# Optimization experiments

Hardware: AMD Instinct MI355X
Metric: run time of the kernel (lower is better)

## Reference

```python
import jax, jax.numpy as jnp
import numpy as np

C = 256
LN_EPS = 1e-5

def setup_inputs() -> dict:
    key = jax.random.key(0)
    ks = jax.random.split(key, 12)
    B, M, N = 8, 4096, 4096
    scale = 1.0 / np.sqrt(C)
    inp = {
        'x': jax.random.normal(ks[0], (B, M, C), jnp.float32),
        'y': jax.random.normal(ks[1], (B, N, C), jnp.float32),
        'Wq': jax.random.normal(ks[2], (C, C), jnp.float32) * scale,
        'bq': jnp.zeros((C,), jnp.float32),
        'Wk': jax.random.normal(ks[3], (C, C), jnp.float32) * scale,
        'bk': jnp.zeros((C,), jnp.float32),
        'Wv': jax.random.normal(ks[4], (C, C), jnp.float32) * scale,
        'bv': jnp.zeros((C,), jnp.float32),
        'Wo': jax.random.normal(ks[5], (C, C), jnp.float32) * (scale * 1e-5),
        'bo': jnp.zeros((C,), jnp.float32),
        'gamma': jnp.ones((C,), jnp.float32),
        'beta': jnp.zeros((C,), jnp.float32),
    }
    return inp

def reference(x, y, Wq, bq, Wk, bk, Wv, bv, Wo, bo, gamma, beta):
    # projections (torch Linear: x @ W.T + b)
    q = x @ Wq.T + bq                      # [B,M,C]
    k = y @ Wk.T + bk                      # [B,N,C]
    v = y @ Wv.T + bv                      # [B,N,C]
    # scaled dot-product attention with explicit score matrix
    w = jnp.einsum('bmc,bnc->bmn', q, k) * (C ** -0.5)  # [B,M,N]
    w = jax.nn.softmax(w, axis=-1)
    h = jnp.einsum('bmn,bnc->bmc', w, v)   # [B,M,C]
    h = h @ Wo.T + bo
    z = x + h
    # LayerNorm over last dim
    mu = jnp.mean(z, axis=-1, keepdims=True)
    var = jnp.var(z, axis=-1, keepdims=True)
    out = (z - mu) * jax.lax.rsqrt(var + LN_EPS) * gamma + beta
    return out
```

## Files before the change

### kernel.cpp

```cpp
#include <hip/hip_runtime.h>
#include <hip/hip_bf16.h>

#define C_DIM 256
#define QSCALE 0.09016844f
#define SM_BIAS -6.0f
#define WO_SCALE 1048576.0f
#define WO_INV   9.5367431640625e-07f

typedef __attribute__((ext_vector_type(8))) short bf16x8;
typedef __attribute__((ext_vector_type(4))) float f32x4;
typedef __attribute__((ext_vector_type(16))) float f32x16;

__device__ __forceinline__ void gload16(const unsigned char* g, unsigned char* l) {
    __builtin_amdgcn_global_load_lds(
        (const __attribute__((address_space(1))) void*)g,
        (__attribute__((address_space(3))) void*)l, 16, 0, 0);
}

__global__ void cvt_w_kernel(const float* __restrict__ w0, const float* __restrict__ w1,
                             const float* __restrict__ w2, const float* __restrict__ w3,
                             unsigned char* __restrict__ o0, unsigned char* __restrict__ o1,
                             unsigned char* __restrict__ o2, unsigned char* __restrict__ o3) {
    int i = (blockIdx.x * 256 + threadIdx.x) * 4;
    #pragma unroll
    for (int wsel = 0; wsel < 4; ++wsel) {
        const float* w = wsel == 0 ? w0 : (wsel == 1 ? w1 : (wsel == 2 ? w2 : w3));
        unsigned char* o = wsel == 0 ? o0 : (wsel == 1 ? o1 : (wsel == 2 ? o2 : o3));
        const float sc = (wsel == 3) ? WO_SCALE : 1.0f;
        float4 v = *reinterpret_cast<const float4*>(w + i);
        unsigned p = __builtin_amdgcn_cvt_pk_fp8_f32(v.x * sc, v.y * sc, 0, false);
        p = __builtin_amdgcn_cvt_pk_fp8_f32(v.z * sc, v.w * sc, p, true);
        *reinterpret_cast<unsigned*>(o + i) = p;
    }
}

__global__ __launch_bounds__(256, 1)
void proj_kernel(const float* __restrict__ x, const float* __restrict__ y,
                 const unsigned char* __restrict__ wq8, const unsigned char* __restrict__ wk8,
                 const unsigned char* __restrict__ wv8,
                 const float* __restrict__ bqp, const float* __restrict__ bkp,
                 const float* __restrict__ bvp,
                 unsigned char* __restrict__ qo, unsigned char* __restrict__ ko,
                 unsigned char* __restrict__ vo)
{
    __shared__ __align__(16) unsigned char ldsW[65536];
    __shared__ __align__(16) unsigned char ldsA[32768];

    const int which = blockIdx.x >> 8;
    const int tile = blockIdx.x & 255;
    const float* in = (which == 0) ? x : y;
    const unsigned char* wsrc = (which == 0) ? wq8 : (which == 1 ? wk8 : wv8);
    const float* bias = (which == 0) ? bqp : (which == 1 ? bkp : bvp);
    unsigned char* out = (which == 0) ? qo : (which == 1 ? ko : vo);
    const float oscale = (which == 0) ? QSCALE : 1.0f;

    const int tid = threadIdx.x;
    const int rowbase = tile * 128;

    #pragma unroll
    for (int it = 0; it < 16; ++it) {
        int G = it * 256 + tid;
        int c = G >> 4, p = G & 15;
        gload16(wsrc + c * 256 + ((p ^ (c & 15)) << 4), ldsW + G * 16);
    }
    #pragma unroll
    for (int it = 0; it < 32; ++it) {
        int e = it * 1024 + tid * 4;
        int r = e >> 8, c4 = e & 255;
        float4 v = *reinterpret_cast<const float4*>(in + (size_t)(rowbase + r) * C_DIM + c4);
        unsigned p = __builtin_amdgcn_cvt_pk_fp8_f32(v.x, v.y, 0, false);
        p = __builtin_amdgcn_cvt_pk_fp8_f32(v.z, v.w, p, true);
        int g = (c4 >> 4) ^ (r & 15);
        *reinterpret_cast<unsigned*>(ldsA + r * 256 + g * 16 + (c4 & 12)) = p;
    }
    __syncthreads();

    const int lane = tid & 63, wave = tid >> 6;
    const int lrow = lane & 15, lkq = lane >> 4;
    const int koff = (lkq & 1) << 3;
    const int kg = lkq >> 1;

    #pragma unroll
    for (int ms = 0; ms < 2; ++ms) {
        const int arow = wave * 32 + ms * 16 + lrow;
        long a[8];
        #pragma unroll
        for (int ks = 0; ks < 8; ++ks)
            a[ks] = *reinterpret_cast<const long*>(
                ldsA + arow * 256 + (((ks * 2 + kg) ^ (arow & 15)) << 4) + koff);

        f32x4 acc[16];
        #pragma unroll
        for (int nf = 0; nf < 16; ++nf) acc[nf] = f32x4{0.f, 0.f, 0.f, 0.f};

        #pragma unroll
        for (int nf = 0; nf < 16; ++nf) {
            const int c = nf * 16 + lrow;
            const unsigned char* wb = ldsW + c * 256;
            const int cx = c & 15;
            #pragma unroll
            for (int ks = 0; ks < 8; ++ks) {
                long b = *reinterpret_cast<const long*>(wb + (((ks * 2 + kg) ^ cx) << 4) + koff);
                acc[nf] = __builtin_amdgcn_mfma_f32_16x16x32_fp8_fp8(a[ks], b, acc[nf], 0, 0, 0);
            }
        }

        const int base = rowbase + wave * 32 + ms * 16 + lkq * 4;
        if (which != 2) {
            const int rsw = (which == 1) ? (base & 8) : 0;
            #pragma unroll
            for (int nf = 0; nf < 16; ++nf) {
                float bv = bias[nf * 16 + lrow];
                float v0 = (acc[nf][0] + bv) * oscale, v1 = (acc[nf][1] + bv) * oscale;
                float v2 = (acc[nf][2] + bv) * oscale, v3 = (acc[nf][3] + bv) * oscale;
                unsigned p = __builtin_amdgcn_cvt_pk_fp8_f32(v0, v1, 0, false);
                p = __builtin_amdgcn_cvt_pk_fp8_f32(v2, v3, p, true);
                int col = (nf * 16 + lrow) ^ rsw;
                unsigned char* o = out + (size_t)base * C_DIM + col;
                o[0]   = (unsigned char)p;
                o[256] = (unsigned char)(p >> 8);
                o[512] = (unsigned char)(p >> 16);
                o[768] = (unsigned char)(p >> 24);
            }
        } else {
            int bb = base >> 12, n0 = base & 4095;
            #pragma unroll
            for (int nf = 0; nf < 16; ++nf) {
                float bv = bias[nf * 16 + lrow];
                float v0 = acc[nf][0] + bv, v1 = acc[nf][1] + bv;
                float v2 = acc[nf][2] + bv, v3 = acc[nf][3] + bv;
                unsigned p = __builtin_amdgcn_cvt_pk_fp8_f32(v0, v1, 0, false);
                p = __builtin_amdgcn_cvt_pk_fp8_f32(v2, v3, p, true);
                int c = nf * 16 + lrow;
                *reinterpret_cast<unsigned*>(vo + ((size_t)bb * C_DIM + c) * 4096 + (n0 ^ (c & 8))) = p;
            }
        }
    }
}

__global__ __launch_bounds__(512, 1)
void attn_kernel(const unsigned char* __restrict__ qg, const unsigned char* __restrict__ kg,
                 const unsigned char* __restrict__ vtg, unsigned short* __restrict__ hg)
{
    __shared__ __align__(16) unsigned char smb[98304];

    const int tid = threadIdx.x;
    const int lane = tid & 63;
    const int w = tid >> 6;
    const int wq = w & 3;
    const int half = w >> 2;
    const int l31 = lane & 31;
    const int hi5 = lane >> 5;
    const int ksw = l31 & 15;
    const int hsw = ((l31 >> 3) & 1) << 3;
    const int vsw = ((l31 >> 2) & 1);

    const int batch = blockIdx.x & 7;
    const int mt = blockIdx.x >> 3;
    const size_t q0 = (size_t)batch * 4096 + mt * 128 + wq * 32;

    const unsigned char* kbase = kg + ((size_t)batch * 4096 + half * 2048) * 256;
    const unsigned char* vbase = vtg + (size_t)batch * 256 * 4096 + half * 2048;

    long qf[16];
    #pragma unroll
    for (int ks = 0; ks < 16; ++ks)
        qf[ks] = *reinterpret_cast<const long*>(qg + (q0 + l31) * 256 + ks * 16 + hi5 * 8);

    f32x16 o[8];
    #pragma unroll
    for (int cb = 0; cb < 8; ++cb) {
        #pragma unroll
        for (int r = 0; r < 16; ++r) o[cb][r] = 0.f;
    }

    float lsum = 0.f;

    auto stage = [&](int buf, int kt) {
        const int kv0 = kt * 32;
        unsigned char* lk = smb + (half * 2 + buf) * 8192;
        unsigned char* lv = smb + 32768 + (half * 2 + buf) * 8192;
        #pragma unroll
        for (int i = 0; i < 2; ++i) {
            int g = wq * 128 + i * 64 + lane;
            int row = g >> 4, pos = g & 15;
            gload16(kbase + (size_t)(kv0 + row) * 256 + ((pos ^ (row & 15)) << 4), lk + g * 16);
        }
        #pragma unroll
        for (int i = 0; i < 2; ++i) {
            int s = wq * 128 + i * 64 + lane;
            int c = s >> 1;
            int k2 = (s & 1) ^ ((s >> 3) & 1);
            gload16(vbase + (size_t)c * 4096 + kv0 + k2 * 16, lv + s * 16);
        }
    };

    auto do_S = [&](int kb, f32x16& sreg) {
        const unsigned char* krow = smb + (half * 2 + kb) * 8192 + l31 * 256 + ((hi5 * 8) ^ hsw);
        #pragma unroll
        for (int r = 0; r < 16; ++r) sreg[r] = SM_BIAS;
        __builtin_amdgcn_s_setprio(1);
        #pragma unroll
        for (int ks = 0; ks < 16; ++ks) {
            long a0 = *reinterpret_cast<const long*>(krow + ((ks ^ ksw) << 4));
            sreg = __builtin_amdgcn_mfma_f32_32x32x16_fp8_fp8(a0, qf[ks], sreg, 0, 0, 0);
        }
        __builtin_amdgcn_s_setprio(0);
    };

    auto do_SM = [&](f32x16& sreg, long& pb0, long& pb1) {
        float ts = 0.f;
        #pragma unroll
        for (int r = 0; r < 16; ++r) { sreg[r] = exp2f(sreg[r]); ts += sreg[r]; }
        ts += __shfl_xor(ts, 32, 64);
        lsum += ts;

        unsigned Wu[4];
        #pragma unroll
        for (int a = 0; a < 4; ++a) {
            unsigned p = __builtin_amdgcn_cvt_pk_fp8_f32(sreg[4 * a], sreg[4 * a + 1], 0, false);
            Wu[a] = __builtin_amdgcn_cvt_pk_fp8_f32(sreg[4 * a + 2], sreg[4 * a + 3], p, true);
        }

        const bool h = (hi5 != 0);
        #pragma unroll
        for (int ksv = 0; ksv < 2; ++ksv) {
            unsigned snd = h ? Wu[2 * ksv] : Wu[2 * ksv + 1];
            unsigned rcv = __shfl_xor(snd, 32, 64);
            unsigned wlo = h ? rcv : Wu[2 * ksv];
            unsigned whi = h ? Wu[2 * ksv + 1] : rcv;
            long pb = (long)(((unsigned long long)whi << 32) | (unsigned long long)wlo);
            if (ksv == 0) pb0 = pb; else pb1 = pb;
        }
    };

    auto do_PV = [&](long pb0, long pb1, int vb) {
        const unsigned char* vrow = smb + 32768 + (half * 2 + vb) * 8192
                                    + l31 * 32 + ((hi5 * 8) ^ hsw);
        __builtin_amdgcn_s_setprio(1);
        #pragma unroll
        for (int ksv = 0; ksv < 2; ++ksv) {
            const int k2s = (ksv ^ vsw) << 4;
            #pragma unroll
            for (int cb = 0; cb < 8; ++cb) {
                long vf = *reinterpret_cast<const long*>(vrow + cb * 1024 + k2s);
                o[cb] = __builtin_amdgcn_mfma_f32_32x32x16_fp8_fp8(
                    vf, ksv ? pb1 : pb0, o[cb], 0, 0, 0);
            }
        }
        __builtin_amdgcn_s_setprio(0);
    };

    stage(0, 0);
    __syncthreads();

    f32x16 s0;
    long pb0 = 0, pb1 = 0;

    for (int kt = 0; kt < 64; ++kt) {
        const int cur = kt & 1;
        if (kt < 63) stage(cur ^ 1, kt + 1);
        do_S(cur, s0);
        do_SM(s0, pb0, pb1);
        do_PV(pb0, pb1, cur);
        __syncthreads();
    }

    unsigned short* pub = (unsigned short*)smb;
    float* ml = (float*)(smb + 90112);

    if (half == 1) {
        if (hi5 == 0) ml[wq * 32 + l31] = lsum;
        unsigned short* prow = pub + (wq * 32 + l31) * 256;
        const int cxor = (l31 & 15) << 2;
        #pragma unroll
        for (int cb = 0; cb < 8; ++cb) {
            #pragma unroll
            for (int rp = 0; rp < 8; ++rp) {
                const int r = 2 * rp;
                unsigned wpk;
                float lo = o[cb][r], hi_ = o[cb][r + 1];
                asm("v_cvt_pk_bf16_f32 %0, %1, %2" : "=v"(wpk) : "v"(lo), "v"(hi_));
                int c = cb * 32 + (r & 3) + 8 * (r >> 2) + 4 * hi5;
                *reinterpret_cast<unsigned*>(prow + (c ^ cxor)) = wpk;
            }
        }
    }
    __syncthreads();

    if (half == 0) {
        float l1 = ml[wq * 32 + l31];
        float rinv = 1.0f / (lsum + l1);

        const unsigned short* prow = pub + (wq * 32 + l31) * 256;
        const int cxor = (l31 & 15) << 2;
        unsigned short* tr = (unsigned short*)(smb + 65536 + wq * 4608);
        #pragma unroll
        for (int cc = 0; cc < 4; ++cc) {
            #pragma unroll
            for (int cbh = 0; cbh < 2; ++cbh) {
                const int cb = cc * 2 + cbh;
                #pragma unroll
                for (int rp = 0; rp < 8; ++rp) {
                    const int r = 2 * rp;
                    int c = cb * 32 + (r & 3) + 8 * (r >> 2) + 4 * hi5;
                    unsigned pk = *reinterpret_cast<const unsigned*>(prow + (c ^ cxor));
                    union { unsigned u; float f; } b0u, b1u;
                    b0u.u = pk << 16; b1u.u = pk & 0xffff0000u;
                    float v_lo = (o[cb][r]     + b0u.f) * rinv;
                    float v_hi = (o[cb][r + 1] + b1u.f) * rinv;
                    unsigned wpk;
                    asm("v_cvt_pk_bf16_f32 %0, %1, %2" : "=v"(wpk) : "v"(v_lo), "v"(v_hi));
                    int c_local = 32 * cbh + (r & 3) + 8 * (r >> 2) + 4 * hi5;
                    *reinterpret_cast<unsigned*>(tr + l31 * 72 + c_local) = wpk;
                }
            }
            __builtin_amdgcn_s_waitcnt(0);
            #pragma unroll
            for (int i = 0; i < 4; ++i) {
                int idx = i * 64 + lane;
                int q = idx >> 3, ch = idx & 7;
                uint4 d = *reinterpret_cast<const uint4*>(tr + q * 72 + ch * 8);
                *reinterpret_cast<uint4*>(hg + (q0 + q) * 256 + cc * 64 + ch * 8) = d;
            }
        }
    }
}

__global__ __launch_bounds__(256, 1)
void out_kernel(const unsigned short* __restrict__ hb, const unsigned char* __restrict__ wo8,
                const float* __restrict__ bo, const float* __restrict__ xg,
                const float* __restrict__ gamma, const float* __restrict__ beta,
                float* __restrict__ outg)
{
    __shared__ __align__(16) unsigned char ldsW[65536];
    __shared__ __align__(16) unsigned char ldsA[32768];

    const int tid = threadIdx.x;
    const int rowbase = blockIdx.x * 128;

    #pragma unroll
    for (int it = 0; it < 16; ++it) {
        int G = it * 256 + tid;
        int c = G >> 4, p = G & 15;
        gload16(wo8 + c * 256 + ((p ^ (c & 15)) << 4), ldsW + G * 16);
    }
    #pragma unroll
    for (int it = 0; it < 16; ++it) {
        int e = it * 2048 + tid * 8;
        int r = e >> 8, c8 = e & 255;
        uint4 d = *reinterpret_cast<const uint4*>(hb + (size_t)(rowbase + r) * C_DIM + c8);
        union { unsigned u; float f; } f0, f1, f2, f3, f4, f5, f6, f7;
        f0.u = d.x << 16; f1.u = d.x & 0xffff0000u;
        f2.u = d.y << 16; f3.u = d.y & 0xffff0000u;
        f4.u = d.z << 16; f5.u = d.z & 0xffff0000u;
        f6.u = d.w << 16; f7.u = d.w & 0xffff0000u;
        unsigned p0 = __builtin_amdgcn_cvt_pk_fp8_f32(f0.f, f1.f, 0, false);
        p0 = __builtin_amdgcn_cvt_pk_fp8_f32(f2.f, f3.f, p0, true);
        unsigned p1 = __builtin_amdgcn_cvt_pk_fp8_f32(f4.f, f5.f, 0, false);
        p1 = __builtin_amdgcn_cvt_pk_fp8_f32(f6.f, f7.f, p1, true);
        int g = (c8 >> 4) ^ (r & 15);
        uint2 pk; pk.x = p0; pk.y = p1;
        *reinterpret_cast<uint2*>(ldsA + r * 256 + g * 16 + (c8 & 8)) = pk;
    }
    __syncthreads();

    const int lane = tid & 63, wave = tid >> 6;
    const int lrow = lane & 15, lkq = lane >> 4;
    const int koff = (lkq & 1) << 3;
    const int kg = lkq >> 1;

    #pragma unroll
    for (int ms = 0; ms < 2; ++ms) {
        const int arow = wave * 32 + ms * 16 + lrow;
        long a[8];
        #pragma unroll
        for (int ks = 0; ks < 8; ++ks)
            a[ks] = *reinterpret_cast<const long*>(
                ldsA + arow * 256 + (((ks * 2 + kg) ^ (arow & 15)) << 4) + koff);

        f32x4 acc[16];
        #pragma unroll
        for (int nf = 0; nf < 16; ++nf) acc[nf] = f32x4{0.f, 0.f, 0.f, 0.f};

        #pragma unroll
        for (int nf = 0; nf < 16; ++nf) {
            const int c = nf * 16 + lrow;
            const unsigned char* wb = ldsW + c * 256;
            const int cx = c & 15;
            #pragma unroll
            for (int ks = 0; ks < 8; ++ks) {
                long b = *reinterpret_cast<const long*>(wb + (((ks * 2 + kg) ^ cx) << 4) + koff);
                acc[nf] = __builtin_amdgcn_mfma_f32_16x16x32_fp8_fp8(a[ks], b, acc[nf], 0, 0, 0);
            }
        }

        const int base = rowbase + wave * 32 + ms * 16 + lkq * 4;

        #pragma unroll
        for (int nf = 0; nf < 16; ++nf) {
            float bv = bo[nf * 16 + lrow];
            #pragma unroll
            for (int r = 0; r < 4; ++r) {
                size_t row = base + r;
                acc[nf][r] = acc[nf][r] * WO_INV + bv + xg[row * C_DIM + nf * 16 + lrow];
            }
        }

        float mu[4], rstd[4];
        #pragma unroll
        for (int r = 0; r < 4; ++r) {
            float s1 = 0.f, s2 = 0.f;
            #pragma unroll
            for (int nf = 0; nf < 16; ++nf) { float v = acc[nf][r]; s1 += v; s2 += v * v; }
            #pragma unroll
            for (int off = 1; off < 16; off <<= 1) {
                s1 += __shfl_xor(s1, off, 64);
                s2 += __shfl_xor(s2, off, 64);
            }
            float m = s1 * (1.f / 256.f);
            mu[r] = m;
            rstd[r] = rsqrtf(s2 * (1.f / 256.f) - m * m + 1e-5f);
        }

        #pragma unroll
        for (int nf = 0; nf < 16; ++nf) {
            float g = gamma[nf * 16 + lrow];
            float bt = beta[nf * 16 + lrow];
            #pragma unroll
            for (int r = 0; r < 4; ++r) {
                size_t row = base + r;
                outg[row * C_DIM + nf * 16 + lrow] = (acc[nf][r] - mu[r]) * rstd[r] * g + bt;
            }
        }
    }
}

extern "C" void kernel_launch(void* const* d_in, const int* in_sizes, int n_in,
                              void* d_out, int out_size, void* d_ws, size_t ws_size,
                              hipStream_t stream) {
    const float* x     = (const float*)d_in[0];
    const float* y     = (const float*)d_in[1];
    const float* Wq    = (const float*)d_in[2];
    const float* bq    = (const float*)d_in[3];
    const float* Wk    = (const float*)d_in[4];
    const float* bk    = (const float*)d_in[5];
    const float* Wv    = (const float*)d_in[6];
    const float* bv    = (const float*)d_in[7];
    const float* Wo    = (const float*)d_in[8];
    const float* bo    = (const float*)d_in[9];
    const float* gamma = (const float*)d_in[10];
    const float* beta  = (const float*)d_in[11];
    float* out = (float*)d_out;

    unsigned char* ws = (unsigned char*)d_ws;
    unsigned char* wq8 = ws;
    unsigned char* wk8 = ws + 65536;
    unsigned char* wv8 = ws + 131072;
    unsigned char* wo8 = ws + 196608;
    unsigned char* q_b = ws + 262144;
    unsigned char* k_b = q_b + 8388608;
    unsigned char* v_b = k_b + 8388608;
    unsigned short* h_b = (unsigned short*)(v_b + 8388608);

    cvt_w_kernel<<<64, 256, 0, stream>>>(Wq, Wk, Wv, Wo, wq8, wk8, wv8, wo8);

    proj_kernel<<<768, 256, 0, stream>>>(x, y, wq8, wk8, wv8, bq, bk, bv, q_b, k_b, v_b);

    attn_kernel<<<256, 512, 0, stream>>>(q_b, k_b, v_b, h_b);

    out_kernel<<<256, 256, 0, stream>>>(h_b, wo8, bo, x, gamma, beta, out);
}
```

Measured before the change: 181.3 us.

## Use 32x32x64 scaled FP8 MFMA for PV with 64-key double-buffered tiles

The PV product now uses the gfx950 mfma_scale 32x32x64 f8f6f4 instruction in place of pairs of 32x32x16 fp8 MFMAs. To fill its 64-wide K dimension, each iteration stages 64 keys (two 32-key subtiles) instead of 32, so the shared buffer grows to 128KB and the V^T layout loses its XOR swizzle. Softmax probabilities for the two subtiles are packed into an 8-dword B operand. The aim is fewer MFMA issues and fewer barriers per key, at the cost of more LDS, more registers and possible bank conflicts on the unswizzled V reads.

```diff
diff --git a/kernel.cpp b/kernel.cpp
--- a/kernel.cpp
+++ b/kernel.cpp
@@ -10,6 +10,7 @@
 typedef __attribute__((ext_vector_type(8))) short bf16x8;
 typedef __attribute__((ext_vector_type(4))) float f32x4;
 typedef __attribute__((ext_vector_type(16))) float f32x16;
+typedef __attribute__((ext_vector_type(8))) int i32x8;
 
 __device__ __forceinline__ void gload16(const unsigned char* g, unsigned char* l) {
     __builtin_amdgcn_global_load_lds(
@@ -132,7 +133,7 @@
                 unsigned p = __builtin_amdgcn_cvt_pk_fp8_f32(v0, v1, 0, false);
                 p = __builtin_amdgcn_cvt_pk_fp8_f32(v2, v3, p, true);
                 int c = nf * 16 + lrow;
-                *reinterpret_cast<unsigned*>(vo + ((size_t)bb * C_DIM + c) * 4096 + (n0 ^ (c & 8))) = p;
+                *reinterpret_cast<unsigned*>(vo + ((size_t)bb * C_DIM + c) * 4096 + n0) = p;
             }
         }
     }
@@ -142,7 +143,7 @@
 void attn_kernel(const unsigned char* __restrict__ qg, const unsigned char* __restrict__ kg,
                  const unsigned char* __restrict__ vtg, unsigned short* __restrict__ hg)
 {
-    __shared__ __align__(16) unsigned char smb[98304];
+    __shared__ __align__(16) unsigned char smb[131072];
 
     const int tid = threadIdx.x;
     const int lane = tid & 63;
@@ -153,7 +154,6 @@
     const int hi5 = lane >> 5;
     const int ksw = l31 & 15;
     const int hsw = ((l31 >> 3) & 1) << 3;
-    const int vsw = ((l31 >> 2) & 1);
 
     const int batch = blockIdx.x & 7;
     const int mt = blockIdx.x >> 3;
@@ -176,27 +176,28 @@
 
     float lsum = 0.f;
 
-    auto stage = [&](int buf, int kt) {
-        const int kv0 = kt * 32;
-        unsigned char* lk = smb + (half * 2 + buf) * 8192;
-        unsigned char* lv = smb + 32768 + (half * 2 + buf) * 8192;
-        #pragma unroll
-        for (int i = 0; i < 2; ++i) {
-            int g = wq * 128 + i * 64 + lane;
-            int row = g >> 4, pos = g & 15;
-            gload16(kbase + (size_t)(kv0 + row) * 256 + ((pos ^ (row & 15)) << 4), lk + g * 16);
-        }
-        #pragma unroll
-        for (int i = 0; i < 2; ++i) {
-            int s = wq * 128 + i * 64 + lane;
-            int c = s >> 1;
-            int k2 = (s & 1) ^ ((s >> 3) & 1);
-            gload16(vbase + (size_t)c * 4096 + kv0 + k2 * 16, lv + s * 16);
+    auto stage = [&](int buf, int rt) {
+        const int kv0 = rt * 64;
+        #pragma unroll
+        for (int i = 0; i < 4; ++i) {
+            int g = wq * 256 + i * 64 + lane;
+            int sub = g >> 9, gs = g & 511;
+            int row = gs >> 4, pos = gs & 15;
+            gload16(kbase + (size_t)(kv0 + sub * 32 + row) * 256 + ((pos ^ (row & 15)) << 4),
+                    smb + (half * 4 + buf * 2 + sub) * 8192 + gs * 16);
+        }
+        #pragma unroll
+        for (int i = 0; i < 4; ++i) {
+            int s = wq * 256 + i * 64 + lane;
+            int sub = s >> 9, ss = s & 511;
+            int k2 = ss >> 8, c = ss & 255;
+            gload16(vbase + (size_t)c * 4096 + kv0 + sub * 32 + k2 * 16,
+                    smb + 65536 + (half * 4 + buf * 2 + sub) * 8192 + ss * 16);
         }
     };
 
-    auto do_S = [&](int kb, f32x16& sreg) {
-        const unsigned char* krow = smb + (half * 2 + kb) * 8192 + l31 * 256 + ((hi5 * 8) ^ hsw);
+    auto do_S = [&](int kidx, f32x16& sreg) {
+        const unsigned char* krow = smb + kidx * 8192 + l31 * 256 + ((hi5 * 8) ^ hsw);
         #pragma unroll
         for (int r = 0; r < 16; ++r) sreg[r] = SM_BIAS;
         __builtin_amdgcn_s_setprio(1);
@@ -208,7 +209,7 @@
         __builtin_amdgcn_s_setprio(0);
     };
 
-    auto do_SM = [&](f32x16& sreg, long& pb0, long& pb1) {
+    auto do_SM = [&](f32x16& sreg, unsigned* pvB, int sub) {
         float ts = 0.f;
         #pragma unroll
         for (int r = 0; r < 16; ++r) { sreg[r] = exp2f(sreg[r]); ts += sreg[r]; }
@@ -221,32 +222,33 @@
             unsigned p = __builtin_amdgcn_cvt_pk_fp8_f32(sreg[4 * a], sreg[4 * a + 1], 0, false);
             Wu[a] = __builtin_amdgcn_cvt_pk_fp8_f32(sreg[4 * a + 2], sreg[4 * a + 3], p, true);
         }
-
-        const bool h = (hi5 != 0);
-        #pragma unroll
-        for (int ksv = 0; ksv < 2; ++ksv) {
-            unsigned snd = h ? Wu[2 * ksv] : Wu[2 * ksv + 1];
-            unsigned rcv = __shfl_xor(snd, 32, 64);
-            unsigned wlo = h ? rcv : Wu[2 * ksv];
-            unsigned whi = h ? Wu[2 * ksv + 1] : rcv;
-            long pb = (long)(((unsigned long long)whi << 32) | (unsigned long long)wlo);
-            if (ksv == 0) pb0 = pb; else pb1 = pb;
+        unsigned rcv[4];
+        #pragma unroll
+        for (int a = 0; a < 4; ++a) rcv[a] = __shfl_xor(Wu[a], 32, 64);
+
+        const bool own = (hi5 == sub);
+        #pragma unroll
+        for (int a = 0; a < 4; ++a) {
+            unsigned lo = hi5 ? rcv[a] : Wu[a];
+            unsigned hi = hi5 ? Wu[a] : rcv[a];
+            pvB[2 * a]     = own ? lo : pvB[2 * a];
+            pvB[2 * a + 1] = own ? hi : pvB[2 * a + 1];
         }
     };
 
-    auto do_PV = [&](long pb0, long pb1, int vb) {
-        const unsigned char* vrow = smb + 32768 + (half * 2 + vb) * 8192
-                                    + l31 * 32 + ((hi5 * 8) ^ hsw);
+    auto do_PV = [&](const unsigned* pvB, int b0) {
+        union { unsigned u[8]; i32x8 v; } B;
+        #pragma unroll
+        for (int j = 0; j < 8; ++j) B.u[j] = pvB[j];
+        const unsigned char* va = smb + 65536 + (b0 + hi5) * 8192 + l31 * 16;
         __builtin_amdgcn_s_setprio(1);
         #pragma unroll
-        for (int ksv = 0; ksv < 2; ++ksv) {
-            const int k2s = (ksv ^ vsw) << 4;
-            #pragma unroll
-            for (int cb = 0; cb < 8; ++cb) {
-                long vf = *reinterpret_cast<const long*>(vrow + cb * 1024 + k2s);
-                o[cb] = __builtin_amdgcn_mfma_f32_32x32x16_fp8_fp8(
-                    vf, ksv ? pb1 : pb0, o[cb], 0, 0, 0);
-            }
+        for (int cb = 0; cb < 8; ++cb) {
+            union { uint4 u4[2]; i32x8 v; } A;
+            A.u4[0] = *reinterpret_cast<const uint4*>(va + cb * 512);
+            A.u4[1] = *reinterpret_cast<const uint4*>(va + cb * 512 + 4096);
+            o[cb] = __builtin_amdgcn_mfma_scale_f32_32x32x64_f8f6f4(
+                A.v, B.v, o[cb], 0, 0, 0, 0x7f7f7f7f, 0, 0x7f7f7f7f);
         }
         __builtin_amdgcn_s_setprio(0);
     };
@@ -255,14 +257,21 @@
     __syncthreads();
 
     f32x16 s0;
-    long pb0 = 0, pb1 = 0;
-
-    for (int kt = 0; kt < 64; ++kt) {
-        const int cur = kt & 1;
-        if (kt < 63) stage(cur ^ 1, kt + 1);
-        do_S(cur, s0);
-        do_SM(s0, pb0, pb1);
-        do_PV(pb0, pb1, cur);
+    unsigned pvB[8];
+    #pragma unroll
+    for (int j = 0; j < 8; ++j) pvB[j] = 0;
+
+    for (int rt = 0; rt < 32; ++rt) {
+        const int cur = rt & 1;
+        if (rt < 31) stage(cur ^ 1, rt + 1);
+        const int b0 = half * 4 + cur * 2;
+
+        do_S(b0, s0);
+        do_SM(s0, pvB, 0);
+        do_S(b0 + 1, s0);
+        do_SM(s0, pvB, 1);
+        do_PV(pvB, b0);
+
         __syncthreads();
     }
 
```

Result: slower. 225.9 us (+24.6%).
